# Performance work log

Hardware: AMD Instinct MI355X
Metric: run time of the kernel (lower is better)

## Reference

```python
import jax, jax.numpy as jnp
import numpy as np


def _mish(x):
    return x * jnp.tanh(jax.nn.softplus(x))


def setup_inputs() -> dict:
    key = jax.random.key(0)
    ks = jax.random.split(key, 10)
    N, D, U, NB, M, MD = 2048, 1024, 2048, 4, 8192, 1024
    g = lambda k, shape, s=0.02: jax.random.normal(k, shape, jnp.float32) * s
    return dict(
        x=jax.random.normal(ks[0], (N, D), jnp.float32),
        w=g(ks[1], (D, U, NB)),
        delay=g(ks[2], (D, U, NB)),
        b=jnp.zeros((U, NB), jnp.float32),
        gate_W=g(ks[3], (D, NB)),
        gate_b=jnp.zeros((NB,), jnp.float32),
        neuron_avg=jax.random.uniform(ks[4], (U,), jnp.float32),
        conn_W1=g(ks[5], (U, 32)),
        conn_b1=jnp.zeros((32,), jnp.float32),
        conn_W2=g(ks[6], (32, U)),
        conn_b2=jnp.zeros((U,), jnp.float32),
        mask=jnp.ones((U,), jnp.float32),
        act_w=jnp.ones((9,), jnp.float32),
        read_W=g(ks[7], (U, M)),
        read_b=jnp.zeros((M,), jnp.float32),
        memory=g(ks[8], (M, MD), 1.0),
    )


def reference(x, w, delay, b, gate_W, gate_b, neuron_avg, conn_W1, conn_b1,
              conn_W2, conn_b2, mask, act_w, read_W, read_b, memory):
    # --- DynamicPlasticDenseDendritic forward ---
    w_mod = w * jax.nn.sigmoid(delay)                      # [D,U,NB]
    branch = jnp.einsum('nd,dub->nub', x, w_mod) + b       # [N,U,NB]
    gate = jax.nn.softmax(x @ gate_W + gate_b, axis=-1)    # [N,NB]
    z = jnp.einsum('nub,nb->nu', branch, gate)             # [N,U]
    # DynamicConnectivity on neuron activation averages (single row)
    h = jax.nn.relu(neuron_avg[None, :] @ conn_W1 + conn_b1)   # [1,32]
    conn = jax.nn.sigmoid(h @ conn_W2 + conn_b2)               # [1,U]
    a = jax.nn.relu(z * conn * mask[None, :])                  # [N,U]
    # --- LearnedActivation: softmax-weighted 8-way activation blend (+zero) ---
    wts = jax.nn.softmax(act_w)
    blend = (wts[0] * jax.nn.sigmoid(a) + wts[1] * jax.nn.elu(a)
             + wts[2] * jnp.tanh(a) + wts[3] * jax.nn.relu(a)
             + wts[4] * jax.nn.silu(a) + wts[5] * jax.nn.gelu(a, approximate=False)
             + wts[6] * jax.nn.selu(a) + wts[7] * _mish(a))
    # --- EpisodicMemory read ---
    attn = jax.nn.softmax(blend @ read_W + read_b, axis=-1)   # [N,M]
    read = attn @ memory                                       # [N,MD]
    return read
```

## Files before the change

kernel.cpp:

```cpp
#include <hip/hip_runtime.h>


typedef unsigned short u16;
typedef __attribute__((ext_vector_type(8))) short bf16x8;
typedef __attribute__((ext_vector_type(4))) float f32x4;

__device__ __forceinline__ float b2f(u16 h) {
    union { unsigned u; float f; } v; v.u = ((unsigned)h) << 16; return v.f;
}
__device__ __forceinline__ u16 f2b(float f) {
    union { float f; unsigned u; } v; v.f = f;
    unsigned u = v.u;
    return (u16)((u + 0x7fffu + ((u >> 16) & 1u)) >> 16);
}

__device__ __forceinline__ void async_copy16(void* lds, const void* g) {
    __builtin_amdgcn_global_load_lds(
        (__attribute__((address_space(1))) void*)(g),
        (__attribute__((address_space(3))) void*)(lds), 16, 0, 0);
}

__device__ __forceinline__ int swz(int o) { return o ^ (((o >> 7) & 7) << 4); }

__device__ __forceinline__ int swz64(int kg, int row) { return kg ^ (row & 3); }

__device__ __forceinline__ void stage_tile256(const u16* __restrict__ src, int ld,
                                              int base0, int k0,
                                              char* ldsbase, int tid)
{
#pragma unroll
    for (int h = 0; h < 2; h++)
#pragma unroll
        for (int it = 0; it < 2; it++) {
            int o = it * 8192 + tid * 16;
            int s = swz(o);
            int r = s >> 7;
            int c = (s & 127) >> 1;
            async_copy16(ldsbase + h * 16384 + o,
                         src + (size_t)(base0 + h * 128 + r) * ld + k0 + c);
        }
}

__device__ __forceinline__ void gemm256_core8(const u16* __restrict__ A,
                                              const u16* __restrict__ B,
                                              int Ktiles, int ld,
                                              int row0, int col0,
                                              char* lds, f32x4 (&acc)[8][4])
{
    const int tid  = threadIdx.x;
    const int lane = tid & 63;
    const int wv   = tid >> 6;
    const int wr   = wv >> 2;
    const int wc   = wv & 3;
    const int lr   = lane & 15, kg = lane >> 4;

#pragma unroll
    for (int i = 0; i < 8; i++)
#pragma unroll
        for (int j = 0; j < 4; j++) {
            f32x4 z = {0.f, 0.f, 0.f, 0.f};
            acc[i][j] = z;
        }

    stage_tile256(A, ld, row0, 0, lds, tid);
    stage_tile256(B, ld, col0, 0, lds + 32768, tid);
    asm volatile("s_waitcnt vmcnt(0)" ::: "memory");
    __builtin_amdgcn_s_barrier();

    bf16x8 af03[4][2], af47[4][2], bfr[2][2];

    for (int t = 0; t < Ktiles; t++) {
        const int buf = (t & 1) << 16;
        const char* sA = lds + buf + wr * 16384;
        const char* sB = lds + buf + 32768 + ((wc >> 1) * 16384);
        char* nb = lds + (((t + 1) & 1) << 16);
        const bool pf = (t + 1 < Ktiles);

        auto rdA = [&](int i, int ks) {
            int off = (i * 16 + lr) * 128 + ks * 64 + kg * 16;
            return *(const bf16x8*)(sA + swz(off));
        };
        auto rdB = [&](int j, int ks) {
            int off = ((wc & 1) * 64 + j * 16 + lr) * 128 + ks * 64 + kg * 16;
            return *(const bf16x8*)(sB + swz(off));
        };

#pragma unroll
        for (int i = 0; i < 4; i++) { af03[i][0] = rdA(i, 0); af03[i][1] = rdA(i, 1); }
#pragma unroll
        for (int j = 0; j < 2; j++) { bfr[j][0] = rdB(j, 0); bfr[j][1] = rdB(j, 1); }
        if (pf) stage_tile256(A, ld, row0, (t + 1) * 64, nb, tid);
        __builtin_amdgcn_s_barrier();
        __builtin_amdgcn_s_setprio(1);
#pragma unroll
        for (int i = 0; i < 4; i++)
#pragma unroll
            for (int j = 0; j < 2; j++) {
                acc[i][j] = __builtin_amdgcn_mfma_f32_16x16x32_bf16(af03[i][0], bfr[j][0], acc[i][j], 0, 0, 0);
                acc[i][j] = __builtin_amdgcn_mfma_f32_16x16x32_bf16(af03[i][1], bfr[j][1], acc[i][j], 0, 0, 0);
            }
        __builtin_amdgcn_s_setprio(0);
        __builtin_amdgcn_s_barrier();

#pragma unroll
        for (int i = 0; i < 4; i++) { af47[i][0] = rdA(4 + i, 0); af47[i][1] = rdA(4 + i, 1); }
        if (pf) stage_tile256(B, ld, col0, (t + 1) * 64, nb + 32768, tid);
        __builtin_amdgcn_s_barrier();
        __builtin_amdgcn_s_setprio(1);
#pragma unroll
        for (int i = 0; i < 4; i++)
#pragma unroll
            for (int j = 0; j < 2; j++) {
                acc[4 + i][j] = __builtin_amdgcn_mfma_f32_16x16x32_bf16(af47[i][0], bfr[j][0], acc[4 + i][j], 0, 0, 0);
                acc[4 + i][j] = __builtin_amdgcn_mfma_f32_16x16x32_bf16(af47[i][1], bfr[j][1], acc[4 + i][j], 0, 0, 0);
            }
        __builtin_amdgcn_s_setprio(0);
        __builtin_amdgcn_s_barrier();

#pragma unroll
        for (int j = 0; j < 2; j++) { bfr[j][0] = rdB(2 + j, 0); bfr[j][1] = rdB(2 + j, 1); }
        __builtin_amdgcn_s_barrier();
        __builtin_amdgcn_s_setprio(1);
#pragma unroll
        for (int i = 0; i < 4; i++)
#pragma unroll
            for (int j = 0; j < 2; j++) {
                acc[4 + i][2 + j] = __builtin_amdgcn_mfma_f32_16x16x32_bf16(af47[i][0], bfr[j][0], acc[4 + i][2 + j], 0, 0, 0);
                acc[4 + i][2 + j] = __builtin_amdgcn_mfma_f32_16x16x32_bf16(af47[i][1], bfr[j][1], acc[4 + i][2 + j], 0, 0, 0);
            }
        __builtin_amdgcn_s_setprio(0);
        __builtin_amdgcn_s_barrier();

        __builtin_amdgcn_s_setprio(1);
#pragma unroll
        for (int i = 0; i < 4; i++)
#pragma unroll
            for (int j = 0; j < 2; j++) {
                acc[i][2 + j] = __builtin_amdgcn_mfma_f32_16x16x32_bf16(af03[i][0], bfr[j][0], acc[i][2 + j], 0, 0, 0);
                acc[i][2 + j] = __builtin_amdgcn_mfma_f32_16x16x32_bf16(af03[i][1], bfr[j][1], acc[i][2 + j], 0, 0, 0);
            }
        __builtin_amdgcn_s_setprio(0);
        asm volatile("s_waitcnt vmcnt(0)" ::: "memory");
        __builtin_amdgcn_s_barrier();
    }
}

template<int BM, int BN, int S>
__device__ __forceinline__ void gemm_core_db(const u16* __restrict__ A,
                                             const u16* __restrict__ B,
                                             int Kloop, int ld,
                                             int row0, int col0,
                                             u16* smem,
                                             f32x4 (&acc)[BM / 32][BN / 32])
{
    constexpr int MT = BM / 32, NT = BN / 32;
    constexpr int STG = (BM + BN) * 32;
    constexpr int SET = STG * S;
    const int tid  = threadIdx.x;
    const int lane = tid & 63;
    const int wv   = tid >> 6;
    const int wr   = wv >> 1, wc = wv & 1;
    const int lr   = lane & 15, kg = lane >> 4;

#pragma unroll
    for (int i = 0; i < MT; i++)
#pragma unroll
        for (int j = 0; j < NT; j++) {
            f32x4 z = {0.f, 0.f, 0.f, 0.f};
            acc[i][j] = z;
        }

    auto stage_in = [&](u16* set, int k0) {
#pragma unroll
        for (int c = tid; c < BM * 4; c += 256) {
            int row = c >> 2, sl = swz64(c & 3, row);
            const u16* gA = A + (size_t)(row0 + row) * ld + k0 + sl * 8;
#pragma unroll
            for (int s = 0; s < S; s++)
                async_copy16(set + s * STG + c * 8, gA + s * 32);
        }
#pragma unroll
        for (int c = tid; c < BN * 4; c += 256) {
            int row = c >> 2, sl = swz64(c & 3, row);
            const u16* gB = B + (size_t)(col0 + row) * ld + k0 + sl * 8;
#pragma unroll
            for (int s = 0; s < S; s++)
                async_copy16(set + s * STG + BM * 32 + c * 8, gB + s * 32);
        }
    };

    stage_in(smem, 0);
    __syncthreads();

    int p = 0;
    for (int k0 = 0; k0 < Kloop; k0 += 32 * S) {
        if (k0 + 32 * S < Kloop)
            stage_in(smem + (p ^ 1) * SET, k0 + 32 * S);
        u16* set = smem + p * SET;
#pragma unroll
        for (int s = 0; s < S; s++) {
            const u16* sA = set + s * STG;
            const u16* sB = sA + BM * 32;
            bf16x8 af[MT], bfr[NT];
#pragma unroll
            for (int i = 0; i < MT; i++) {
                int row = wr * (BM / 2) + i * 16 + lr;
                af[i] = *(const bf16x8*)(sA + (row * 32 + swz64(kg, row) * 8));
            }
#pragma unroll
            for (int j = 0; j < NT; j++) {
                int row = wc * (BN / 2) + j * 16 + lr;
                bfr[j] = *(const bf16x8*)(sB + (row * 32 + swz64(kg, row) * 8));
            }
#pragma unroll
            for (int i = 0; i < MT; i++)
#pragma unroll
                for (int j = 0; j < NT; j++)
                    acc[i][j] = __builtin_amdgcn_mfma_f32_16x16x32_bf16(
                                    af[i], bfr[j], acc[i][j], 0, 0, 0);
        }
        __syncthreads();
        p ^= 1;
    }
}

__global__ __launch_bounds__(256)
void k_small(const float* __restrict__ na, const float* __restrict__ W1,
             const float* __restrict__ b1, const float* __restrict__ W2,
             const float* __restrict__ b2, const float* __restrict__ actw,
             float* __restrict__ conn, float* __restrict__ wts)
{
    __shared__ float red[256 * 32];
    __shared__ float hsh[32];
    const int tid = threadIdx.x;
    float h[32];
#pragma unroll
    for (int k = 0; k < 32; k++) h[k] = 0.f;
    for (int u = tid; u < 2048; u += 256) {
        float nav = na[u];
        const float* row = W1 + u * 32;
#pragma unroll
        for (int k = 0; k < 32; k++) h[k] += nav * row[k];
    }
#pragma unroll
    for (int k = 0; k < 32; k++) red[tid * 32 + k] = h[k];
    for (int s = 128; s > 0; s >>= 1) {
        __syncthreads();
        if (tid < s)
#pragma unroll
            for (int k = 0; k < 32; k++) red[tid * 32 + k] += red[(tid + s) * 32 + k];
    }
    __syncthreads();
    if (tid < 32) hsh[tid] = fmaxf(red[tid] + b1[tid], 0.f);
    if (tid == 0) {
        float e[9], m = -1e30f;
        for (int i = 0; i < 9; i++) { e[i] = actw[i]; m = fmaxf(m, e[i]); }
        float s = 0.f;
        for (int i = 0; i < 9; i++) { e[i] = expf(e[i] - m); s += e[i]; }
        for (int i = 0; i < 9; i++) wts[i] = e[i] / s;
    }
    __syncthreads();
    for (int u = tid; u < 2048; u += 256) {
        float a = 0.f;
#pragma unroll
        for (int k = 0; k < 32; k++) a += hsh[k] * W2[k * 2048 + u];
        conn[u] = 1.f / (1.f + expf(-(a + b2[u])));
    }
}

__global__ __launch_bounds__(256)
void k_gate_y(const float* __restrict__ x, const float* __restrict__ gW,
              const float* __restrict__ gb, float* __restrict__ gate,
              u16* __restrict__ y)
{
    const int tid = threadIdx.x, lane = tid & 63, wv = tid >> 6;
    const int n = blockIdx.x * 4 + wv;
    const float* xr = x + (size_t)n * 1024;
    float a0 = 0, a1 = 0, a2 = 0, a3 = 0;
    float xv[16];
#pragma unroll
    for (int s = 0; s < 16; s++) {
        int d = s * 64 + lane;
        float xd = xr[d]; xv[s] = xd;
        float4 g4 = *(const float4*)(gW + d * 4);
        a0 += xd * g4.x; a1 += xd * g4.y; a2 += xd * g4.z; a3 += xd * g4.w;
    }
#pragma unroll
    for (int off = 32; off > 0; off >>= 1) {
        a0 += __shfl_xor(a0, off); a1 += __shfl_xor(a1, off);
        a2 += __shfl_xor(a2, off); a3 += __shfl_xor(a3, off);
    }
    a0 += gb[0]; a1 += gb[1]; a2 += gb[2]; a3 += gb[3];
    float m = fmaxf(fmaxf(a0, a1), fmaxf(a2, a3));
    float e0 = expf(a0 - m), e1 = expf(a1 - m), e2 = expf(a2 - m), e3 = expf(a3 - m);
    float inv = 1.f / (e0 + e1 + e2 + e3);
    float g0 = e0 * inv, g1 = e1 * inv, g2 = e2 * inv, g3 = e3 * inv;
    if (lane == 0) *(float4*)(gate + n * 4) = make_float4(g0, g1, g2, g3);
#pragma unroll
    for (int s = 0; s < 16; s++) {
        int d = s * 64 + lane;
        ushort4 o;
        o.x = f2b(xv[s] * g0); o.y = f2b(xv[s] * g1);
        o.z = f2b(xv[s] * g2); o.w = f2b(xv[s] * g3);
        *(ushort4*)(y + (size_t)n * 4096 + d * 4) = o;
    }
}

__global__ __launch_bounds__(256)
void k_wmT(const float* __restrict__ w, const float* __restrict__ delay,
           u16* __restrict__ wmT)
{
    __shared__ __align__(16) ushort4 tile[32][65];
    const int tid = threadIdx.x;
    const int tx = tid & 63, ty = tid >> 6;
    const int u0 = blockIdx.x * 64, d0 = blockIdx.y * 32;
#pragma unroll
    for (int i = 0; i < 8; i++) {
        int d = i * 4 + ty;
        size_t idx = ((size_t)(d0 + d) * 2048 + (u0 + tx)) * 4;
        float4 w4 = *(const float4*)(w + idx);
        float4 d4 = *(const float4*)(delay + idx);
        ushort4 o;
        o.x = f2b(w4.x / (1.f + expf(-d4.x)));
        o.y = f2b(w4.y / (1.f + expf(-d4.y)));
        o.z = f2b(w4.z / (1.f + expf(-d4.z)));
        o.w = f2b(w4.w / (1.f + expf(-d4.w)));
        tile[d][tx] = o;
    }
    __syncthreads();
    const int dx = tid & 31, uy = tid >> 5;
#pragma unroll
    for (int i = 0; i < 8; i++) {
        int u = i * 8 + uy;
        *(ushort4*)(wmT + (size_t)(u0 + u) * 4096 + (d0 + dx) * 4) = tile[dx][u];
    }
}

__global__ __launch_bounds__(256)
void k_transpose(const float* __restrict__ in, u16* __restrict__ out, int R, int C)
{
    __shared__ __align__(16) u16 t[64][68];
    const int tid = threadIdx.x, tx = tid & 15, ty = tid >> 4;
    const int c0 = blockIdx.x * 64, r0 = blockIdx.y * 64;
#pragma unroll
    for (int i = 0; i < 4; i++) {
        int r = r0 + ty + i * 16;
        float4 v = *(const float4*)(in + (size_t)r * C + c0 + tx * 4);
        t[tx * 4 + 0][ty + i * 16] = f2b(v.x); t[tx * 4 + 1][ty + i * 16] = f2b(v.y);
        t[tx * 4 + 2][ty + i * 16] = f2b(v.z); t[tx * 4 + 3][ty + i * 16] = f2b(v.w);
    }
    __syncthreads();
#pragma unroll
    for (int i = 0; i < 4; i++) {
        int c = ty + i * 16;
        ushort4 v;
        v.x = t[c][tx * 4 + 0]; v.y = t[c][tx * 4 + 1];
        v.z = t[c][tx * 4 + 2]; v.w = t[c][tx * 4 + 3];
        *(ushort4*)(out + (size_t)(c0 + c) * R + r0 + tx * 4) = v;
    }
}

__device__ __forceinline__ float act_blend(float a,
    float w0, float w1, float w2, float w3,
    float w4, float w5, float w6, float w7)
{
    float sig = 1.f / (1.f + expf(-a));
    float elu = (a > 0.f) ? a : (expf(a) - 1.f);
    float th  = tanhf(a);
    float rel = fmaxf(a, 0.f);
    float sil = a * sig;
    float gel = a * 0.5f * (1.f + erff(a * 0.70710678118654752f));
    float sel = (a > 0.f) ? 1.0507009873554805f * a
                          : 1.0507009873554805f * 1.6732632423543772f * (expf(a) - 1.f);
    float sp  = (a > 20.f) ? a : log1pf(expf(a));
    float mish = a * tanhf(sp);
    return w0 * sig + w1 * elu + w2 * th + w3 * rel + w4 * sil + w5 * gel
         + w6 * sel + w7 * mish;
}

__global__ __launch_bounds__(512, 2)
void k_gemm_a8(const u16* __restrict__ A, const u16* __restrict__ B,
               float* __restrict__ P)
{
    __shared__ __align__(16) char lds[131072];
    const int row0 = blockIdx.y * 256, col0 = blockIdx.x * 256;
    const u16* Ac = A + (size_t)blockIdx.z * 1024;
    const u16* Bc = B + (size_t)blockIdx.z * 1024;

    f32x4 acc[8][4];
    gemm256_core8(Ac, Bc, 16, 4096, row0, col0, lds, acc);

    float* Pz = P + (size_t)blockIdx.z * 2048 * 2048;
    const int tid = threadIdx.x, lane = tid & 63, wv = tid >> 6;
    const int wr = wv >> 2, wc = wv & 3, lr = lane & 15, kg = lane >> 4;
#pragma unroll
    for (int i = 0; i < 8; i++)
#pragma unroll
        for (int r = 0; r < 4; r++) {
            int n = row0 + wr * 128 + i * 16 + kg * 4 + r;
            size_t ob = (size_t)n * 2048;
#pragma unroll
            for (int j = 0; j < 4; j++)
                Pz[ob + col0 + wc * 64 + j * 16 + lr] = acc[i][j][r];
        }
}

__global__ __launch_bounds__(256)
void k_reduce_blend(const float* __restrict__ P, const float* __restrict__ gate,
                    const float* __restrict__ conn, const float* __restrict__ mask,
                    const float* __restrict__ wts, const float* __restrict__ bbias,
                    u16* __restrict__ blend)
{
    constexpr size_t SL = (size_t)2048 * 2048;
    const int n  = blockIdx.x;
    const int u0 = threadIdx.x * 8;
    const float* base = P + (size_t)n * 2048 + u0;

    float v[8];
#pragma unroll
    for (int h = 0; h < 2; h++) {
        float4 a = *(const float4*)(base + h * 4);
        float4 b = *(const float4*)(base + SL + h * 4);
        float4 c = *(const float4*)(base + 2 * SL + h * 4);
        float4 d = *(const float4*)(base + 3 * SL + h * 4);
        v[h * 4 + 0] = a.x + b.x + c.x + d.x;
        v[h * 4 + 1] = a.y + b.y + c.y + d.y;
        v[h * 4 + 2] = a.z + b.z + c.z + d.z;
        v[h * 4 + 3] = a.w + b.w + c.w + d.w;
    }
    float4 g = *(const float4*)(gate + n * 4);
    const float w0 = wts[0], w1 = wts[1], w2 = wts[2], w3 = wts[3];
    const float w4 = wts[4], w5 = wts[5], w6 = wts[6], w7 = wts[7];

    ushort4 o[2];
#pragma unroll
    for (int j = 0; j < 8; j++) {
        int u = u0 + j;
        float4 b4 = *(const float4*)(bbias + u * 4);
        float z = v[j] + g.x * b4.x + g.y * b4.y + g.z * b4.z + g.w * b4.w;
        float a = fmaxf(z * conn[u] * mask[u], 0.f);
        u16 r = f2b(act_blend(a, w0, w1, w2, w3, w4, w5, w6, w7));
        ((u16*)o)[j] = r;
    }
    *(ushort4*)(blend + (size_t)n * 2048 + u0)     = o[0];
    *(ushort4*)(blend + (size_t)n * 2048 + u0 + 4) = o[1];
}

__global__ __launch_bounds__(512, 2)
void k_gemm_logits8(const u16* __restrict__ BL, const u16* __restrict__ RWT,
                    const float* __restrict__ rbias, u16* __restrict__ out)
{
    __shared__ __align__(16) char lds[131072];
    const int row0 = blockIdx.y * 256, col0 = blockIdx.x * 256;

    f32x4 acc[8][4];
    gemm256_core8(BL, RWT, 32, 2048, row0, col0, lds, acc);

    const int tid = threadIdx.x, lane = tid & 63, wv = tid >> 6;
    const int wr = wv >> 2, wc = wv & 3, lr = lane & 15, kg = lane >> 4;
    float rb[4]; int mm[4];
#pragma unroll
    for (int j = 0; j < 4; j++) {
        mm[j] = col0 + wc * 64 + j * 16 + lr;
        rb[j] = rbias[mm[j]];
    }
#pragma unroll
    for (int i = 0; i < 8; i++)
#pragma unroll
        for (int r = 0; r < 4; r++) {
            int n = row0 + wr * 128 + i * 16 + kg * 4 + r;
            size_t ob = (size_t)n * 8192;
#pragma unroll
            for (int j = 0; j < 4; j++)
                out[ob + mm[j]] = f2b(acc[i][j][r] + rb[j]);
        }
}

__global__ __launch_bounds__(256)
void k_softmax(u16* __restrict__ buf)
{
    __shared__ float red[8];
    const int tid = threadIdx.x, lane = tid & 63, wv = tid >> 6;
    u16* row = buf + (size_t)blockIdx.x * 8192;
    float v[32];
    float mx = -1e30f;
#pragma unroll
    for (int s = 0; s < 8; s++) {
        ushort4 u4 = *(const ushort4*)(row + (s * 256 + tid) * 4);
        float a = b2f(u4.x), b = b2f(u4.y), c = b2f(u4.z), d = b2f(u4.w);
        v[s * 4 + 0] = a; v[s * 4 + 1] = b; v[s * 4 + 2] = c; v[s * 4 + 3] = d;
        mx = fmaxf(mx, fmaxf(fmaxf(a, b), fmaxf(c, d)));
    }
#pragma unroll
    for (int off = 32; off > 0; off >>= 1) mx = fmaxf(mx, __shfl_xor(mx, off));
    if (lane == 0) red[wv] = mx;
    __syncthreads();
    mx = fmaxf(fmaxf(red[0], red[1]), fmaxf(red[2], red[3]));
    float sum = 0.f;
#pragma unroll
    for (int k = 0; k < 32; k++) { v[k] = expf(v[k] - mx); sum += v[k]; }
#pragma unroll
    for (int off = 32; off > 0; off >>= 1) sum += __shfl_xor(sum, off);
    if (lane == 0) red[4 + wv] = sum;
    __syncthreads();
    float inv = 1.f / (red[4] + red[5] + red[6] + red[7]);
#pragma unroll
    for (int s = 0; s < 8; s++) {
        ushort4 o;
        o.x = f2b(v[s * 4 + 0] * inv); o.y = f2b(v[s * 4 + 1] * inv);
        o.z = f2b(v[s * 4 + 2] * inv); o.w = f2b(v[s * 4 + 3] * inv);
        *(ushort4*)(row + (s * 256 + tid) * 4) = o;
    }
}

template<int BM, int BN, int S, int NCOL>
__global__ __launch_bounds__(256, 4)
void k_gemm_partial(const u16* __restrict__ A, const u16* __restrict__ B,
                    int Kchunk, int ld, float* __restrict__ P)
{
    constexpr int MT = BM / 32, NT = BN / 32;
    __shared__ __align__(16) u16 smem[2 * (BM + BN) * 32 * S];

    const int nx = gridDim.x, ny = gridDim.y;
    const int f  = blockIdx.x + nx * blockIdx.y;
    const int ch = (nx * ny) >> 3;
    const int sw = (f & 7) * ch + (f >> 3);
    const int bx = sw % nx, by = sw / nx;
    const int row0 = by * BM, col0 = bx * BN;

    const u16* Ac = A + (size_t)blockIdx.z * Kchunk;
    const u16* Bc = B + (size_t)blockIdx.z * Kchunk;

    f32x4 acc[MT][NT];
    gemm_core_db<BM, BN, S>(Ac, Bc, Kchunk, ld, row0, col0, smem, acc);

    float* Pz = P + (size_t)blockIdx.z * 2048 * NCOL;
    const int tid = threadIdx.x, lane = tid & 63, wv = tid >> 6;
    const int wr = wv >> 1, wc = wv & 1, lr = lane & 15, kg = lane >> 4;
#pragma unroll
    for (int i = 0; i < MT; i++)
#pragma unroll
        for (int r = 0; r < 4; r++) {
            int n = row0 + wr * (BM / 2) + i * 16 + kg * 4 + r;
            size_t ob = (size_t)n * NCOL;
#pragma unroll
            for (int j = 0; j < NT; j++)
                Pz[ob + col0 + wc * (BN / 2) + j * 16 + lr] = acc[i][j][r];
        }
}

__global__ __launch_bounds__(256)
void k_reduce_out(const float* __restrict__ P, float* __restrict__ out)
{
    constexpr size_t SL = (size_t)2048 * 1024;
    size_t i = ((size_t)blockIdx.x * 256 + threadIdx.x) * 4;
    float4 a = *(const float4*)(P + i);
    float4 b = *(const float4*)(P + SL + i);
    float4 c = *(const float4*)(P + 2 * SL + i);
    float4 d = *(const float4*)(P + 3 * SL + i);
    float4 o;
    o.x = a.x + b.x + c.x + d.x;
    o.y = a.y + b.y + c.y + d.y;
    o.z = a.z + b.z + c.z + d.z;
    o.w = a.w + b.w + c.w + d.w;
    *(float4*)(out + i) = o;
}

__global__ void k_fill(float* out, int n)
{
    int i = blockIdx.x * 256 + threadIdx.x;
    if (i < n) out[i] = 12345.f;
}

extern "C" void kernel_launch(void* const* d_in, const int* in_sizes, int n_in,
                              void* d_out, int out_size, void* d_ws, size_t ws_size,
                              hipStream_t stream)
{
    const float* x     = (const float*)d_in[0];
    const float* w     = (const float*)d_in[1];
    const float* delay = (const float*)d_in[2];
    const float* bb    = (const float*)d_in[3];
    const float* gW    = (const float*)d_in[4];
    const float* gb    = (const float*)d_in[5];
    const float* na    = (const float*)d_in[6];
    const float* cW1   = (const float*)d_in[7];
    const float* cb1   = (const float*)d_in[8];
    const float* cW2   = (const float*)d_in[9];
    const float* cb2   = (const float*)d_in[10];
    const float* mask  = (const float*)d_in[11];
    const float* actw  = (const float*)d_in[12];
    const float* rW    = (const float*)d_in[13];
    const float* rb    = (const float*)d_in[14];
    const float* mem   = (const float*)d_in[15];
    (void)in_sizes; (void)n_in;

    char* ws = (char*)d_ws;
    size_t off = 0;
    auto alloc = [&](size_t bytes) {
        size_t o = off; off += (bytes + 255) & ~(size_t)255; return o;
    };
    size_t o_wts   = alloc(9 * 4);
    size_t o_gate  = alloc(2048 * 4 * 4);
    size_t o_conn  = alloc(2048 * 4);
    size_t o_y     = alloc((size_t)2048 * 4096 * 2);
    size_t o_wmT   = alloc((size_t)2048 * 4096 * 2);
    size_t o_blend = alloc((size_t)2048 * 2048 * 2);
    size_t o_rwT   = alloc((size_t)8192 * 2048 * 2);
    size_t o_log   = alloc((size_t)2048 * 8192 * 2);

    if (off > ws_size) {
        k_fill<<<(out_size + 255) / 256, 256, 0, stream>>>((float*)d_out, out_size);
        return;
    }

    float* wts   = (float*)(ws + o_wts);
    float* gate  = (float*)(ws + o_gate);
    float* conn  = (float*)(ws + o_conn);
    u16* y       = (u16*)(ws + o_y);
    u16* wmT     = (u16*)(ws + o_wmT);
    u16* blend   = (u16*)(ws + o_blend);
    u16* rwT     = (u16*)(ws + o_rwT);
    u16* logits  = (u16*)(ws + o_log);
    u16* memT    = y;

    float* pA = (float*)(ws + o_rwT);
    float* pC = (float*)(ws + o_rwT);

    k_small<<<1, 256, 0, stream>>>(na, cW1, cb1, cW2, cb2, actw, conn, wts);
    k_gate_y<<<512, 256, 0, stream>>>(x, gW, gb, gate, y);
    k_wmT<<<dim3(32, 32), 256, 0, stream>>>(w, delay, wmT);

    k_gemm_a8<<<dim3(8, 8, 4), 512, 0, stream>>>(y, wmT, pA);
    k_reduce_blend<<<2048, 256, 0, stream>>>(pA, gate, conn, mask, wts, bb, blend);

    k_transpose<<<dim3(128, 32), 256, 0, stream>>>(rW, rwT, 2048, 8192);
    k_gemm_logits8<<<dim3(32, 8), 512, 0, stream>>>(blend, rwT, rb, logits);
    k_softmax<<<2048, 256, 0, stream>>>(logits);

    k_transpose<<<dim3(16, 128), 256, 0, stream>>>(mem, memT, 8192, 1024);

    k_gemm_partial<128, 128, 2, 1024><<<dim3(8, 16, 4), 256, 0, stream>>>(
        logits, memT, 2048, 8192, pC);
    k_reduce_out<<<2048, 256, 0, stream>>>(pC, (float*)d_out);
}
```

Before: 432.3 us.

## Merge prep kernels and softmax/transpose launches, trim barriers in 256-tile GEMM

Three small preprocessing kernels (connectivity MLP, gate/y scaling, modulated-weight transpose) become one launch that branches on block index. The row softmax and the memory transpose likewise become one launch using a custom 64x64 transpose path. In the 256x256 GEMM main loop, the second B fragment set is read into its own registers earlier, which removes one barrier pair per K-step at the cost of more live VGPRs. The aim is to cut launch overhead, let independent work run concurrently, and reduce synchronisation, with some risk of register pressure and a heterogeneous block mix.

```diff
diff --git a/kernel.cpp b/kernel.cpp
--- a/kernel.cpp
+++ b/kernel.cpp
@@ -67,7 +67,7 @@
     asm volatile("s_waitcnt vmcnt(0)" ::: "memory");
     __builtin_amdgcn_s_barrier();
 
-    bf16x8 af03[4][2], af47[4][2], bfr[2][2];
+    bf16x8 af03[4][2], af47[4][2], b01[2][2], b23[2][2];
 
     for (int t = 0; t < Ktiles; t++) {
         const int buf = (t & 1) << 16;
@@ -88,7 +88,7 @@
 #pragma unroll
         for (int i = 0; i < 4; i++) { af03[i][0] = rdA(i, 0); af03[i][1] = rdA(i, 1); }
 #pragma unroll
-        for (int j = 0; j < 2; j++) { bfr[j][0] = rdB(j, 0); bfr[j][1] = rdB(j, 1); }
+        for (int j = 0; j < 2; j++) { b01[j][0] = rdB(j, 0); b01[j][1] = rdB(j, 1); }
         if (pf) stage_tile256(A, ld, row0, (t + 1) * 64, nb, tid);
         __builtin_amdgcn_s_barrier();
         __builtin_amdgcn_s_setprio(1);
@@ -96,14 +96,16 @@
         for (int i = 0; i < 4; i++)
 #pragma unroll
             for (int j = 0; j < 2; j++) {
-                acc[i][j] = __builtin_amdgcn_mfma_f32_16x16x32_bf16(af03[i][0], bfr[j][0], acc[i][j], 0, 0, 0);
-                acc[i][j] = __builtin_amdgcn_mfma_f32_16x16x32_bf16(af03[i][1], bfr[j][1], acc[i][j], 0, 0, 0);
+                acc[i][j] = __builtin_amdgcn_mfma_f32_16x16x32_bf16(af03[i][0], b01[j][0], acc[i][j], 0, 0, 0);
+                acc[i][j] = __builtin_amdgcn_mfma_f32_16x16x32_bf16(af03[i][1], b01[j][1], acc[i][j], 0, 0, 0);
             }
         __builtin_amdgcn_s_setprio(0);
         __builtin_amdgcn_s_barrier();
 
 #pragma unroll
         for (int i = 0; i < 4; i++) { af47[i][0] = rdA(4 + i, 0); af47[i][1] = rdA(4 + i, 1); }
+#pragma unroll
+        for (int j = 0; j < 2; j++) { b23[j][0] = rdB(2 + j, 0); b23[j][1] = rdB(2 + j, 1); }
         if (pf) stage_tile256(B, ld, col0, (t + 1) * 64, nb + 32768, tid);
         __builtin_amdgcn_s_barrier();
         __builtin_amdgcn_s_setprio(1);
@@ -111,33 +113,26 @@
         for (int i = 0; i < 4; i++)
 #pragma unroll
             for (int j = 0; j < 2; j++) {
-                acc[4 + i][j] = __builtin_amdgcn_mfma_f32_16x16x32_bf16(af47[i][0], bfr[j][0], acc[4 + i][j], 0, 0, 0);
-                acc[4 + i][j] = __builtin_amdgcn_mfma_f32_16x16x32_bf16(af47[i][1], bfr[j][1], acc[4 + i][j], 0, 0, 0);
+                acc[4 + i][j] = __builtin_amdgcn_mfma_f32_16x16x32_bf16(af47[i][0], b01[j][0], acc[4 + i][j], 0, 0, 0);
+                acc[4 + i][j] = __builtin_amdgcn_mfma_f32_16x16x32_bf16(af47[i][1], b01[j][1], acc[4 + i][j], 0, 0, 0);
             }
         __builtin_amdgcn_s_setprio(0);
         __builtin_amdgcn_s_barrier();
 
-#pragma unroll
-        for (int j = 0; j < 2; j++) { bfr[j][0] = rdB(2 + j, 0); bfr[j][1] = rdB(2 + j, 1); }
-        __builtin_amdgcn_s_barrier();
         __builtin_amdgcn_s_setprio(1);
 #pragma unroll
         for (int i = 0; i < 4; i++)
 #pragma unroll
             for (int j = 0; j < 2; j++) {
-                acc[4 + i][2 + j] = __builtin_amdgcn_mfma_f32_16x16x32_bf16(af47[i][0], bfr[j][0], acc[4 + i][2 + j], 0, 0, 0);
-                acc[4 + i][2 + j] = __builtin_amdgcn_mfma_f32_16x16x32_bf16(af47[i][1], bfr[j][1], acc[4 + i][2 + j], 0, 0, 0);
+                acc[4 + i][2 + j] = __builtin_amdgcn_mfma_f32_16x16x32_bf16(af47[i][0], b23[j][0], acc[4 + i][2 + j], 0, 0, 0);
+                acc[4 + i][2 + j] = __builtin_amdgcn_mfma_f32_16x16x32_bf16(af47[i][1], b23[j][1], acc[4 + i][2 + j], 0, 0, 0);
             }
-        __builtin_amdgcn_s_setprio(0);
-        __builtin_amdgcn_s_barrier();
-
-        __builtin_amdgcn_s_setprio(1);
 #pragma unroll
         for (int i = 0; i < 4; i++)
 #pragma unroll
             for (int j = 0; j < 2; j++) {
-                acc[i][2 + j] = __builtin_amdgcn_mfma_f32_16x16x32_bf16(af03[i][0], bfr[j][0], acc[i][2 + j], 0, 0, 0);
-                acc[i][2 + j] = __builtin_amdgcn_mfma_f32_16x16x32_bf16(af03[i][1], bfr[j][1], acc[i][2 + j], 0, 0, 0);
+                acc[i][2 + j] = __builtin_amdgcn_mfma_f32_16x16x32_bf16(af03[i][0], b23[j][0], acc[i][2 + j], 0, 0, 0);
+                acc[i][2 + j] = __builtin_amdgcn_mfma_f32_16x16x32_bf16(af03[i][1], b23[j][1], acc[i][2 + j], 0, 0, 0);
             }
         __builtin_amdgcn_s_setprio(0);
         asm volatile("s_waitcnt vmcnt(0)" ::: "memory");
@@ -225,114 +220,114 @@
 }
 
 __global__ __launch_bounds__(256)
-void k_small(const float* __restrict__ na, const float* __restrict__ W1,
-             const float* __restrict__ b1, const float* __restrict__ W2,
-             const float* __restrict__ b2, const float* __restrict__ actw,
-             float* __restrict__ conn, float* __restrict__ wts)
-{
-    __shared__ float red[256 * 32];
-    __shared__ float hsh[32];
+void k_prep(const float* __restrict__ na, const float* __restrict__ W1,
+            const float* __restrict__ b1, const float* __restrict__ W2,
+            const float* __restrict__ b2, const float* __restrict__ actw,
+            float* __restrict__ conn, float* __restrict__ wts,
+            const float* __restrict__ x, const float* __restrict__ gW,
+            const float* __restrict__ gb, float* __restrict__ gate,
+            u16* __restrict__ y,
+            const float* __restrict__ w, const float* __restrict__ delay,
+            u16* __restrict__ wmT)
+{
+    __shared__ __align__(16) char sh[256 * 32 * 4 + 128];
+    const int bid = blockIdx.x;
     const int tid = threadIdx.x;
-    float h[32];
-#pragma unroll
-    for (int k = 0; k < 32; k++) h[k] = 0.f;
-    for (int u = tid; u < 2048; u += 256) {
-        float nav = na[u];
-        const float* row = W1 + u * 32;
-#pragma unroll
-        for (int k = 0; k < 32; k++) h[k] += nav * row[k];
-    }
-#pragma unroll
-    for (int k = 0; k < 32; k++) red[tid * 32 + k] = h[k];
-    for (int s = 128; s > 0; s >>= 1) {
+
+    if (bid == 0) {
+        float* red = (float*)sh;
+        float* hsh = (float*)(sh + 256 * 32 * 4);
+        float h[32];
+#pragma unroll
+        for (int k = 0; k < 32; k++) h[k] = 0.f;
+        for (int u = tid; u < 2048; u += 256) {
+            float nav = na[u];
+            const float* row = W1 + u * 32;
+#pragma unroll
+            for (int k = 0; k < 32; k++) h[k] += nav * row[k];
+        }
+#pragma unroll
+        for (int k = 0; k < 32; k++) red[tid * 32 + k] = h[k];
+        for (int s = 128; s > 0; s >>= 1) {
+            __syncthreads();
+            if (tid < s)
+#pragma unroll
+                for (int k = 0; k < 32; k++) red[tid * 32 + k] += red[(tid + s) * 32 + k];
+        }
         __syncthreads();
-        if (tid < s)
-#pragma unroll
-            for (int k = 0; k < 32; k++) red[tid * 32 + k] += red[(tid + s) * 32 + k];
-    }
-    __syncthreads();
-    if (tid < 32) hsh[tid] = fmaxf(red[tid] + b1[tid], 0.f);
-    if (tid == 0) {
-        float e[9], m = -1e30f;
-        for (int i = 0; i < 9; i++) { e[i] = actw[i]; m = fmaxf(m, e[i]); }
-        float s = 0.f;
-        for (int i = 0; i < 9; i++) { e[i] = expf(e[i] - m); s += e[i]; }
-        for (int i = 0; i < 9; i++) wts[i] = e[i] / s;
-    }
-    __syncthreads();
-    for (int u = tid; u < 2048; u += 256) {
-        float a = 0.f;
-#pragma unroll
-        for (int k = 0; k < 32; k++) a += hsh[k] * W2[k * 2048 + u];
-        conn[u] = 1.f / (1.f + expf(-(a + b2[u])));
-    }
-}
-
-__global__ __launch_bounds__(256)
-void k_gate_y(const float* __restrict__ x, const float* __restrict__ gW,
-              const float* __restrict__ gb, float* __restrict__ gate,
-              u16* __restrict__ y)
-{
-    const int tid = threadIdx.x, lane = tid & 63, wv = tid >> 6;
-    const int n = blockIdx.x * 4 + wv;
-    const float* xr = x + (size_t)n * 1024;
-    float a0 = 0, a1 = 0, a2 = 0, a3 = 0;
-    float xv[16];
-#pragma unroll
-    for (int s = 0; s < 16; s++) {
-        int d = s * 64 + lane;
-        float xd = xr[d]; xv[s] = xd;
-        float4 g4 = *(const float4*)(gW + d * 4);
-        a0 += xd * g4.x; a1 += xd * g4.y; a2 += xd * g4.z; a3 += xd * g4.w;
-    }
-#pragma unroll
-    for (int off = 32; off > 0; off >>= 1) {
-        a0 += __shfl_xor(a0, off); a1 += __shfl_xor(a1, off);
-        a2 += __shfl_xor(a2, off); a3 += __shfl_xor(a3, off);
-    }
-    a0 += gb[0]; a1 += gb[1]; a2 += gb[2]; a3 += gb[3];
-    float m = fmaxf(fmaxf(a0, a1), fmaxf(a2, a3));
-    float e0 = expf(a0 - m), e1 = expf(a1 - m), e2 = expf(a2 - m), e3 = expf(a3 - m);
-    float inv = 1.f / (e0 + e1 + e2 + e3);
-    float g0 = e0 * inv, g1 = e1 * inv, g2 = e2 * inv, g3 = e3 * inv;
-    if (lane == 0) *(float4*)(gate + n * 4) = make_float4(g0, g1, g2, g3);
-#pragma unroll
-    for (int s = 0; s < 16; s++) {
-        int d = s * 64 + lane;
-        ushort4 o;
-        o.x = f2b(xv[s] * g0); o.y = f2b(xv[s] * g1);
-        o.z = f2b(xv[s] * g2); o.w = f2b(xv[s] * g3);
-        *(ushort4*)(y + (size_t)n * 4096 + d * 4) = o;
-    }
-}
-
-__global__ __launch_bounds__(256)
-void k_wmT(const float* __restrict__ w, const float* __restrict__ delay,
-           u16* __restrict__ wmT)
-{
-    __shared__ __align__(16) ushort4 tile[32][65];
-    const int tid = threadIdx.x;
-    const int tx = tid & 63, ty = tid >> 6;
-    const int u0 = blockIdx.x * 64, d0 = blockIdx.y * 32;
-#pragma unroll
-    for (int i = 0; i < 8; i++) {
-        int d = i * 4 + ty;
-        size_t idx = ((size_t)(d0 + d) * 2048 + (u0 + tx)) * 4;
-        float4 w4 = *(const float4*)(w + idx);
-        float4 d4 = *(const float4*)(delay + idx);
-        ushort4 o;
-        o.x = f2b(w4.x / (1.f + expf(-d4.x)));
-        o.y = f2b(w4.y / (1.f + expf(-d4.y)));
-        o.z = f2b(w4.z / (1.f + expf(-d4.z)));
-        o.w = f2b(w4.w / (1.f + expf(-d4.w)));
-        tile[d][tx] = o;
-    }
-    __syncthreads();
-    const int dx = tid & 31, uy = tid >> 5;
-#pragma unroll
-    for (int i = 0; i < 8; i++) {
-        int u = i * 8 + uy;
-        *(ushort4*)(wmT + (size_t)(u0 + u) * 4096 + (d0 + dx) * 4) = tile[dx][u];
+        if (tid < 32) hsh[tid] = fmaxf(red[tid] + b1[tid], 0.f);
+        if (tid == 0) {
+            float e[9], m = -1e30f;
+            for (int i = 0; i < 9; i++) { e[i] = actw[i]; m = fmaxf(m, e[i]); }
+            float s = 0.f;
+            for (int i = 0; i < 9; i++) { e[i] = expf(e[i] - m); s += e[i]; }
+            for (int i = 0; i < 9; i++) wts[i] = e[i] / s;
+        }
+        __syncthreads();
+        for (int u = tid; u < 2048; u += 256) {
+            float a = 0.f;
+#pragma unroll
+            for (int k = 0; k < 32; k++) a += hsh[k] * W2[k * 2048 + u];
+            conn[u] = 1.f / (1.f + expf(-(a + b2[u])));
+        }
+    } else if (bid <= 512) {
+        const int lane = tid & 63, wvx = tid >> 6;
+        const int n = (bid - 1) * 4 + wvx;
+        const float* xr = x + (size_t)n * 1024;
+        float a0 = 0, a1 = 0, a2 = 0, a3 = 0;
+        float xv[16];
+#pragma unroll
+        for (int s = 0; s < 16; s++) {
+            int d = s * 64 + lane;
+            float xd = xr[d]; xv[s] = xd;
+            float4 g4 = *(const float4*)(gW + d * 4);
+            a0 += xd * g4.x; a1 += xd * g4.y; a2 += xd * g4.z; a3 += xd * g4.w;
+        }
+#pragma unroll
+        for (int off = 32; off > 0; off >>= 1) {
+            a0 += __shfl_xor(a0, off); a1 += __shfl_xor(a1, off);
+            a2 += __shfl_xor(a2, off); a3 += __shfl_xor(a3, off);
+        }
+        a0 += gb[0]; a1 += gb[1]; a2 += gb[2]; a3 += gb[3];
+        float m = fmaxf(fmaxf(a0, a1), fmaxf(a2, a3));
+        float e0 = expf(a0 - m), e1 = expf(a1 - m), e2 = expf(a2 - m), e3 = expf(a3 - m);
+        float inv = 1.f / (e0 + e1 + e2 + e3);
+        float g0 = e0 * inv, g1 = e1 * inv, g2 = e2 * inv, g3 = e3 * inv;
+        if (lane == 0) *(float4*)(gate + n * 4) = make_float4(g0, g1, g2, g3);
+#pragma unroll
+        for (int s = 0; s < 16; s++) {
+            int d = s * 64 + lane;
+            ushort4 o;
+            o.x = f2b(xv[s] * g0); o.y = f2b(xv[s] * g1);
+            o.z = f2b(xv[s] * g2); o.w = f2b(xv[s] * g3);
+            *(ushort4*)(y + (size_t)n * 4096 + d * 4) = o;
+        }
+    } else {
+        typedef ushort4 row65[65];
+        row65* tile = (row65*)sh;
+        const int b = bid - 513;
+        const int u0 = (b & 31) * 64, d0 = (b >> 5) * 32;
+        const int tx = tid & 63, ty = tid >> 6;
+#pragma unroll
+        for (int i = 0; i < 8; i++) {
+            int d = i * 4 + ty;
+            size_t idx = ((size_t)(d0 + d) * 2048 + (u0 + tx)) * 4;
+            float4 w4 = *(const float4*)(w + idx);
+            float4 d4 = *(const float4*)(delay + idx);
+            ushort4 o;
+            o.x = f2b(w4.x / (1.f + expf(-d4.x)));
+            o.y = f2b(w4.y / (1.f + expf(-d4.y)));
+            o.z = f2b(w4.z / (1.f + expf(-d4.z)));
+            o.w = f2b(w4.w / (1.f + expf(-d4.w)));
+            tile[d][tx] = o;
+        }
+        __syncthreads();
+        const int dx = tid & 31, uy = tid >> 5;
+#pragma unroll
+        for (int i = 0; i < 8; i++) {
+            int u = i * 8 + uy;
+            *(ushort4*)(wmT + (size_t)(u0 + u) * 4096 + (d0 + dx) * 4) = tile[dx][u];
+        }
     }
 }
 
@@ -477,39 +472,68 @@
 }
 
 __global__ __launch_bounds__(256)
-void k_softmax(u16* __restrict__ buf)
-{
-    __shared__ float red[8];
-    const int tid = threadIdx.x, lane = tid & 63, wv = tid >> 6;
-    u16* row = buf + (size_t)blockIdx.x * 8192;
-    float v[32];
-    float mx = -1e30f;
-#pragma unroll
-    for (int s = 0; s < 8; s++) {
-        ushort4 u4 = *(const ushort4*)(row + (s * 256 + tid) * 4);
-        float a = b2f(u4.x), b = b2f(u4.y), c = b2f(u4.z), d = b2f(u4.w);
-        v[s * 4 + 0] = a; v[s * 4 + 1] = b; v[s * 4 + 2] = c; v[s * 4 + 3] = d;
-        mx = fmaxf(mx, fmaxf(fmaxf(a, b), fmaxf(c, d)));
-    }
-#pragma unroll
-    for (int off = 32; off > 0; off >>= 1) mx = fmaxf(mx, __shfl_xor(mx, off));
-    if (lane == 0) red[wv] = mx;
-    __syncthreads();
-    mx = fmaxf(fmaxf(red[0], red[1]), fmaxf(red[2], red[3]));
-    float sum = 0.f;
-#pragma unroll
-    for (int k = 0; k < 32; k++) { v[k] = expf(v[k] - mx); sum += v[k]; }
-#pragma unroll
-    for (int off = 32; off > 0; off >>= 1) sum += __shfl_xor(sum, off);
-    if (lane == 0) red[4 + wv] = sum;
-    __syncthreads();
-    float inv = 1.f / (red[4] + red[5] + red[6] + red[7]);
-#pragma unroll
-    for (int s = 0; s < 8; s++) {
-        ushort4 o;
-        o.x = f2b(v[s * 4 + 0] * inv); o.y = f2b(v[s * 4 + 1] * inv);
-        o.z = f2b(v[s * 4 + 2] * inv); o.w = f2b(v[s * 4 + 3] * inv);
-        *(ushort4*)(row + (s * 256 + tid) * 4) = o;
+void k_post(u16* __restrict__ buf, const float* __restrict__ mem,
+            u16* __restrict__ memT)
+{
+    __shared__ __align__(16) char sh[64 * 68 * 2 + 64];
+    const int bid = blockIdx.x;
+    const int tid = threadIdx.x;
+
+    if (bid < 2048) {
+        float* red = (float*)sh;
+        const int lane = tid & 63, wv = tid >> 6;
+        u16* row = buf + (size_t)bid * 8192;
+        float v[32];
+        float mx = -1e30f;
+#pragma unroll
+        for (int s = 0; s < 8; s++) {
+            ushort4 u4 = *(const ushort4*)(row + (s * 256 + tid) * 4);
+            float a = b2f(u4.x), b = b2f(u4.y), c = b2f(u4.z), d = b2f(u4.w);
+            v[s * 4 + 0] = a; v[s * 4 + 1] = b; v[s * 4 + 2] = c; v[s * 4 + 3] = d;
+            mx = fmaxf(mx, fmaxf(fmaxf(a, b), fmaxf(c, d)));
+        }
+#pragma unroll
+        for (int off = 32; off > 0; off >>= 1) mx = fmaxf(mx, __shfl_xor(mx, off));
+        if (lane == 0) red[wv] = mx;
+        __syncthreads();
+        mx = fmaxf(fmaxf(red[0], red[1]), fmaxf(red[2], red[3]));
+        float sum = 0.f;
+#pragma unroll
+        for (int k = 0; k < 32; k++) { v[k] = expf(v[k] - mx); sum += v[k]; }
+#pragma unroll
+        for (int off = 32; off > 0; off >>= 1) sum += __shfl_xor(sum, off);
+        if (lane == 0) red[4 + wv] = sum;
+        __syncthreads();
+        float inv = 1.f / (red[4] + red[5] + red[6] + red[7]);
+#pragma unroll
+        for (int s = 0; s < 8; s++) {
+            ushort4 o;
+            o.x = f2b(v[s * 4 + 0] * inv); o.y = f2b(v[s * 4 + 1] * inv);
+            o.z = f2b(v[s * 4 + 2] * inv); o.w = f2b(v[s * 4 + 3] * inv);
+            *(ushort4*)(row + (s * 256 + tid) * 4) = o;
+        }
+    } else {
+        typedef u16 row68[68];
+        row68* t = (row68*)sh;
+        const int b = bid - 2048;
+        const int c0 = (b & 15) * 64, r0 = (b >> 4) * 64;
+        const int tx = tid & 15, ty = tid >> 4;
+#pragma unroll
+        for (int i = 0; i < 4; i++) {
+            int r = r0 + ty + i * 16;
+            float4 v = *(const float4*)(mem + (size_t)r * 1024 + c0 + tx * 4);
+            t[tx * 4 + 0][ty + i * 16] = f2b(v.x); t[tx * 4 + 1][ty + i * 16] = f2b(v.y);
+            t[tx * 4 + 2][ty + i * 16] = f2b(v.z); t[tx * 4 + 3][ty + i * 16] = f2b(v.w);
+        }
+        __syncthreads();
+#pragma unroll
+        for (int i = 0; i < 4; i++) {
+            int c = ty + i * 16;
+            ushort4 v;
+            v.x = t[c][tx * 4 + 0]; v.y = t[c][tx * 4 + 1];
+            v.z = t[c][tx * 4 + 2]; v.w = t[c][tx * 4 + 3];
+            *(ushort4*)(memT + (size_t)(c0 + c) * 8192 + r0 + tx * 4) = v;
+        }
     }
 }
 
@@ -626,18 +650,16 @@
     float* pA = (float*)(ws + o_rwT);
     float* pC = (float*)(ws + o_rwT);
 
-    k_small<<<1, 256, 0, stream>>>(na, cW1, cb1, cW2, cb2, actw, conn, wts);
-    k_gate_y<<<512, 256, 0, stream>>>(x, gW, gb, gate, y);
-    k_wmT<<<dim3(32, 32), 256, 0, stream>>>(w, delay, wmT);
+    k_prep<<<1537, 256, 0, stream>>>(na, cW1, cb1, cW2, cb2, actw, conn, wts,
+                                     x, gW, gb, gate, y, w, delay, wmT);
 
     k_gemm_a8<<<dim3(8, 8, 4), 512, 0, stream>>>(y, wmT, pA);
     k_reduce_blend<<<2048, 256, 0, stream>>>(pA, gate, conn, mask, wts, bb, blend);
 
     k_transpose<<<dim3(128, 32), 256, 0, stream>>>(rW, rwT, 2048, 8192);
     k_gemm_logits8<<<dim3(32, 8), 512, 0, stream>>>(blend, rwT, rb, logits);
-    k_softmax<<<2048, 256, 0, stream>>>(logits);
-
-    k_transpose<<<dim3(16, 128), 256, 0, stream>>>(mem, memT, 8192, 1024);
+
+    k_post<<<4096, 256, 0, stream>>>(logits, mem, memT);
 
     k_gemm_partial<128, 128, 2, 1024><<<dim3(8, 16, 4), 256, 0, stream>>>(
         logits, memT, 2048, 8192, pC);
```

Result: slower. 456.1 us (+5.5%).
